# Performance work log

Hardware: AMD Instinct MI355X
Metric: run time of the kernel (lower is better)

The kernel has to match this reference:

```python
import jax, jax.numpy as jnp
import numpy as np

BETA = 0.25  # commitment cost


def setup_inputs() -> dict:
    key = jax.random.key(0)
    k1, k2 = jax.random.split(key)
    z = jax.random.normal(k1, (16, 512, 64, 64), dtype=jnp.float32)       # (B, C=e_dim, H, W)
    codebook = jax.random.normal(k2, (1024, 512), dtype=jnp.float32)      # (n_e, e_dim)
    return {"z": z, "codebook": codebook}


def reference(z, codebook):
    b, c, h, w = z.shape
    zp = jnp.transpose(z, (0, 2, 3, 1))                                   # (B, H, W, C)
    zf = zp.reshape(-1, c)                                                # (N, e_dim)

    d = (jnp.sum(zf * zf, axis=1, keepdims=True)
         + jnp.sum(codebook * codebook, axis=1)
         - 2.0 * (zf @ codebook.T))                                       # (N, n_e)
    idx = jnp.argmin(d, axis=1)                                           # (N,)

    # one-hot @ codebook == direct gather
    z_q = codebook[idx].reshape(zp.shape)                                 # (B, H, W, C)

    sg = jax.lax.stop_gradient
    e_latent_loss = jnp.mean((sg(z_q) - zp) ** 2)
    q_latent_loss = jnp.mean((z_q - sg(zp)) ** 2)
    codebook_loss = q_latent_loss + BETA * e_latent_loss

    # straight-through estimator
    z_q_st = zp + sg(z_q - zp)
    z_q_out = jnp.transpose(z_q_st, (0, 3, 1, 2))                         # (B, C, H, W)
    return z_q_out, codebook_loss, idx.reshape(b, 1, h, w)
```

## Files before the change

### kernel.cpp

```cpp
#include <hip/hip_runtime.h>
#include <hip/hip_bf16.h>


typedef _Float16 h8 __attribute__((ext_vector_type(8)));
typedef float f32x16 __attribute__((ext_vector_type(16)));

#define OUT_LOSS  33554432
#define OUT_IDX   33554433
#define MARGIN_T  0.15f

__device__ __forceinline__ void gload_lds16(const void* g, void* l) {
  __builtin_amdgcn_global_load_lds(
      (const __attribute__((address_space(1))) void*)g,
      (__attribute__((address_space(3))) void*)l, 16, 0, 0);
}

__global__ __launch_bounds__(64) void k0_prep(
    const float* __restrict__ cb, unsigned short* __restrict__ cb16,
    float* __restrict__ cnp, int* __restrict__ counters, float* __restrict__ loss_acc,
    int* __restrict__ idx_ws, unsigned long long* __restrict__ packed_ws)
{
  const int r = blockIdx.x, l = threadIdx.x;
  const float* row = cb + (size_t)r * 512;
  float4 a  = *(const float4*)(row + l * 8);
  float4 b4 = *(const float4*)(row + l * 8 + 4);
  h8 hv;
  hv[0] = (_Float16)a.x;  hv[1] = (_Float16)a.y;  hv[2] = (_Float16)a.z;  hv[3] = (_Float16)a.w;
  hv[4] = (_Float16)b4.x; hv[5] = (_Float16)b4.y; hv[6] = (_Float16)b4.z; hv[7] = (_Float16)b4.w;
  *reinterpret_cast<h8*>(cb16 + (size_t)r * 512 + l * 8) = hv;
  float s = a.x*a.x + a.y*a.y + a.z*a.z + a.w*a.w
          + b4.x*b4.x + b4.y*b4.y + b4.z*b4.z + b4.w*b4.w;
  #pragma unroll
  for (int off = 1; off < 64; off <<= 1) s += __shfl_xor(s, off);
  if (l == 0) {
    int jr = r & 31, ch = r >> 5;
    int khalf = (jr >> 2) & 1;
    int pat = jr - (khalf << 2);
    int rr  = (pat & 3) + ((pat >> 3) << 2);
    cnp[(ch << 5) + (khalf << 4) + rr] = 0.5f * s;
  }
  const int pix = (r << 6) + l;
  idx_ws[pix] = (int)0x80000000;
  packed_ws[pix] = ~0ull;
  if (r == 0 && l == 0) { counters[0] = 0; counters[1] = 0; *loss_acc = 0.f; }
}

__global__ __launch_bounds__(256, 2) void k1_main(
    const float* __restrict__ z, const unsigned short* __restrict__ cb16,
    const float* __restrict__ cnp,
    int* __restrict__ idx_ws, int* __restrict__ flaglist,
    unsigned long long* __restrict__ pairlist, int* __restrict__ counters)
{
  extern __shared__ char smem[];
  float* cn_lds = reinterpret_cast<float*>(smem + 65536);
  const int tid   = threadIdx.x;
  const int lane  = tid & 63;
  const int wave  = tid >> 6;
  const int pxl   = lane & 31;
  const int khalf = lane >> 5;
  const int px0   = blockIdx.x << 7;
  const int b     = px0 >> 12;
  const int hw0   = px0 & 4095;
  const int laneoff = pxl * 1024 + khalf * 16;

  {
    const char* src = reinterpret_cast<const char*>(cb16) + laneoff;
    #pragma unroll
    for (int i = 0; i < 8; ++i) {
      int slab = (wave << 3) + i;
      gload_lds16(src + slab * 32, smem + slab * 1024);
    }
  }

  h8 bfrag[32];
  {
    const float* zl = z + ((size_t)(b * 512 + khalf * 8)) * 4096 + hw0 + (wave << 5) + pxl;
    #pragma unroll
    for (int s = 0; s < 32; ++s) {
      const float* zs = zl + (size_t)s * 16 * 4096;
      h8 hv;
      #pragma unroll
      for (int e = 0; e < 8; ++e) hv[e] = (_Float16)zs[(size_t)e * 4096];
      bfrag[s] = hv;
    }
  }
  for (int i = tid; i < 1024; i += 256) cn_lds[i] = cnp[i];
  __syncthreads();

  float v0 = INFINITY, v1 = INFINITY, v2 = INFINITY, v3 = INFINITY;
  int   i0 = 0, i1 = 0, i2 = 0, i3 = 0;

  for (int ch = 0; ch < 32; ++ch) {
    const char* cbuf = smem + ((ch & 1) << 15);
    if (ch) {
      asm volatile("s_waitcnt vmcnt(0)" ::: "memory");
      __builtin_amdgcn_s_barrier();
    }
    if (ch < 31) {
      char* dbuf = smem + (((ch & 1) ^ 1) << 15);
      const char* src = reinterpret_cast<const char*>(cb16) + ((ch + 1) << 15) + laneoff;
      #pragma unroll
      for (int i = 0; i < 8; ++i) {
        int slab = (wave << 3) + i;
        gload_lds16(src + slab * 32, dbuf + slab * 1024);
      }
    }

    f32x16 acca, accb;
    #pragma unroll
    for (int i = 0; i < 16; ++i) { acca[i] = 0.f; accb[i] = 0.f; }
    {
      const char* ab = cbuf + (pxl << 4) + (khalf << 9);
      #pragma unroll
      for (int s = 0; s < 16; ++s) {
        h8 a0 = *reinterpret_cast<const h8*>(ab + (s << 10));
        h8 a1 = *reinterpret_cast<const h8*>(ab + ((s + 16) << 10));
        acca = __builtin_amdgcn_mfma_f32_32x32x16_f16(a0, bfrag[s],      acca, 0, 0, 0);
        accb = __builtin_amdgcn_mfma_f32_32x32x16_f16(a1, bfrag[s + 16], accb, 0, 0, 0);
      }
    }
    const float* cl = cn_lds + (ch << 5) + (khalf << 4);
    float4 q0 = *(const float4*)(cl);     float4 q1 = *(const float4*)(cl + 4);
    float4 q2 = *(const float4*)(cl + 8); float4 q3 = *(const float4*)(cl + 12);
    const float cn[16] = {q0.x,q0.y,q0.z,q0.w, q1.x,q1.y,q1.z,q1.w,
                          q2.x,q2.y,q2.z,q2.w, q3.x,q3.y,q3.z,q3.w};
    const int jbase = (ch << 5) + (khalf << 2);
    #pragma unroll
    for (int r = 0; r < 16; ++r) {
      int j = jbase + ((r & 3) + ((r >> 2) << 3));
      float sc = cn[r] - (acca[r] + accb[r]);
      if (__ballot(sc < v3)) {
        bool c0 = sc < v0, c1 = sc < v1, c2 = sc < v2, c3 = sc < v3;
        v3 = c2 ? v2 : (c3 ? sc : v3);  i3 = c2 ? i2 : (c3 ? j : i3);
        v2 = c1 ? v1 : (c2 ? sc : v2);  i2 = c1 ? i1 : (c2 ? j : i2);
        v1 = c0 ? v0 : (c1 ? sc : v1);  i1 = c0 ? i0 : (c1 ? j : i1);
        v0 = c0 ? sc : v0;              i0 = c0 ? j  : i0;
      }
    }
  }

  {
    float ow0 = __shfl_xor(v0, 32), ow1 = __shfl_xor(v1, 32),
          ow2 = __shfl_xor(v2, 32), ow3 = __shfl_xor(v3, 32);
    int   oj0 = __shfl_xor(i0, 32), oj1 = __shfl_xor(i1, 32),
          oj2 = __shfl_xor(i2, 32), oj3 = __shfl_xor(i3, 32);
    const float ow[4] = {ow0, ow1, ow2, ow3};
    const int   oj[4] = {oj0, oj1, oj2, oj3};
    #pragma unroll
    for (int k = 0; k < 4; ++k) {
      float ov = ow[k]; int oi = oj[k];
      bool c0 = ov < v0, c1 = ov < v1, c2 = ov < v2, c3 = ov < v3;
      v3 = c2 ? v2 : (c3 ? ov : v3);  i3 = c2 ? i2 : (c3 ? oi : i3);
      v2 = c1 ? v1 : (c2 ? ov : v2);  i2 = c1 ? i1 : (c2 ? oi : i2);
      v1 = c0 ? v0 : (c1 ? ov : v1);  i1 = c0 ? i0 : (c1 ? oi : i1);
      v0 = c0 ? ov : v0;              i0 = c0 ? oi : i0;
    }
  }

  const int pix = px0 + (wave << 5) + lane;
  bool sane = (v0 == v0) && (v3 == v3) && ((unsigned)i0 < 1024u);
  bool unfl = sane && (v1 - v0 >= MARGIN_T);
  bool quad = sane && !unfl && (v3 - v0 >= MARGIN_T);
  bool qpred = (lane < 32) && quad;
  bool fpred = (lane < 32) && !unfl && !quad;
  if (lane < 32) idx_ws[pix] = unfl ? i0 : (int)0x80000000;

  unsigned long long qm = __ballot(qpred);
  if (qm) {
    int leader = __ffsll(qm) - 1;
    int base = 0;
    if (lane == leader) base = atomicAdd(&counters[1], __popcll(qm));
    base = __shfl(base, leader);
    if (qpred) {
      int pos = __popcll(qm & ((1ull << lane) - 1ull));
      pairlist[base + pos] = (unsigned long long)(unsigned)pix
          | ((unsigned long long)(unsigned)i0 << 16)
          | ((unsigned long long)(unsigned)i1 << 26)
          | ((unsigned long long)(unsigned)i2 << 36)
          | ((unsigned long long)(unsigned)i3 << 46);
    }
  }
  unsigned long long fm = __ballot(fpred);
  if (fm) {
    int leader = __ffsll(fm) - 1;
    int base = 0;
    if (lane == leader) base = atomicAdd(&counters[0], __popcll(fm));
    base = __shfl(base, leader);
    if (fpred) {
      int pos = __popcll(fm & ((1ull << lane) - 1ull));
      flaglist[base + pos] = pix;
    }
  }
}

__global__ __launch_bounds__(256) void k2a_quad(
    const float* __restrict__ z, const float* __restrict__ cb,
    const unsigned long long* __restrict__ pairlist, const int* __restrict__ counters,
    int* __restrict__ idx_ws)
{
  const int lane = threadIdx.x & 63;
  const int wid  = (blockIdx.x << 2) + (threadIdx.x >> 6);
  const int nwav = gridDim.x << 2;
  const int nf   = counters[1];
  for (int e = wid; e < nf; e += nwav) {
    unsigned long long pk = pairlist[e];
    int pix = (int)(pk & 0xFFFFull);
    int c0 = (int)((pk >> 16) & 1023ull), c1 = (int)((pk >> 26) & 1023ull);
    int c2 = (int)((pk >> 36) & 1023ull), c3 = (int)((pk >> 46) & 1023ull);
    const float* zp = z + (size_t)(pix >> 12) * 512 * 4096 + (pix & 4095);
    double s0 = 0, s1 = 0, s2 = 0, s3 = 0;
    #pragma unroll
    for (int k = 0; k < 8; ++k) {
      int c = lane + (k << 6);
      double zv2 = 2.0 * (double)zp[(size_t)c * 4096];
      double a;
      a = (double)cb[(size_t)c0 * 512 + c]; s0 = fma(a, a - zv2, s0);
      a = (double)cb[(size_t)c1 * 512 + c]; s1 = fma(a, a - zv2, s1);
      a = (double)cb[(size_t)c2 * 512 + c]; s2 = fma(a, a - zv2, s2);
      a = (double)cb[(size_t)c3 * 512 + c]; s3 = fma(a, a - zv2, s3);
    }
    #pragma unroll
    for (int off = 32; off > 0; off >>= 1) {
      s0 += __shfl_xor(s0, off); s1 += __shfl_xor(s1, off);
      s2 += __shfl_xor(s2, off); s3 += __shfl_xor(s3, off);
    }
    double bv = s0; int bi = c0;
    if (s1 < bv || (s1 == bv && c1 < bi)) { bv = s1; bi = c1; }
    if (s2 < bv || (s2 == bv && c2 < bi)) { bv = s2; bi = c2; }
    if (s3 < bv || (s3 == bv && c3 < bi)) { bv = s3; bi = c3; }
    if (lane == 0) idx_ws[pix] = bi;
  }
}

__global__ __launch_bounds__(256) void k2_rescan(
    const float* __restrict__ z, const float* __restrict__ cb,
    const int* __restrict__ flaglist, const int* __restrict__ counters,
    unsigned long long* __restrict__ packed_ws)
{
  __shared__ float zb[16][512];
  __shared__ unsigned long long best[16];
  __shared__ int pixl[16];
  const int t = threadIdx.x;
  const int nflag = counters[0];
  const int ntasks = ((nflag + 15) >> 4) << 2;
  for (int task = blockIdx.x; task < ntasks; task += gridDim.x) {
    const int g = task >> 2, q = task & 3;
    int rem = nflag - (g << 4);
    const int npx = rem < 16 ? rem : 16;
    if (t < 16) {
      best[t] = ~0ull;
      pixl[t] = (t < npx) ? flaglist[(g << 4) + t] : 0;
    }
    __syncthreads();
    for (int i = t; i < (npx << 9); i += 256) {
      int p = i >> 9, c = i & 511;
      int pix = pixl[p];
      zb[p][c] = z[((size_t)(pix >> 12) * 512 + c) * 4096 + (pix & 4095)];
    }
    __syncthreads();
    const int j = (q << 8) + t;
    const float* row = cb + (size_t)j * 512;
    double dot[16];
    #pragma unroll
    for (int p = 0; p < 16; ++p) dot[p] = 0.0;
    double cn = 0.0;
    for (int k = 0; k < 512; k += 4) {
      float4 cv = *(const float4*)(row + k);
      double c0 = cv.x, c1 = cv.y, c2 = cv.z, c3 = cv.w;
      cn = fma(c0, c0, cn); cn = fma(c1, c1, cn);
      cn = fma(c2, c2, cn); cn = fma(c3, c3, cn);
      #pragma unroll
      for (int p = 0; p < 16; ++p) {
        dot[p] = fma(c0, (double)zb[p][k + 0], dot[p]);
        dot[p] = fma(c1, (double)zb[p][k + 1], dot[p]);
        dot[p] = fma(c2, (double)zb[p][k + 2], dot[p]);
        dot[p] = fma(c3, (double)zb[p][k + 3], dot[p]);
      }
    }
    #pragma unroll
    for (int p = 0; p < 16; ++p) {
      if (p < npx) {
        double d = fma(-2.0, dot[p], cn);
        unsigned long long u = (unsigned long long)__double_as_longlong(d);
        u = (u >> 63) ? ~u : (u | 0x8000000000000000ull);
        unsigned long long pkk = (u & ~1023ull) | (unsigned long long)j;
        atomicMin(&best[p], pkk);
      }
    }
    __syncthreads();
    if (t < npx) atomicMin(&packed_ws[pixl[t]], best[t]);
    __syncthreads();
  }
}

__global__ __launch_bounds__(256) void k3_out(
    const float* __restrict__ z, const float* __restrict__ cb,
    const int* __restrict__ idx_ws, const unsigned long long* __restrict__ packed_ws,
    float* __restrict__ out, float* __restrict__ loss_acc)
{
  extern __shared__ float rows[];
  __shared__ int idxs[32];
  __shared__ float wsum[4];
  const int t = threadIdx.x;
  const int pix0 = blockIdx.x << 5;
  const int b = pix0 >> 12, hw0 = pix0 & 4095;
  if (t < 32) {
    int pix = pix0 + t;
    int v = idx_ws[pix];
    unsigned j = (v < 0) ? (unsigned)(packed_ws[pix] & 1023ull) : (unsigned)v;
    j &= 1023u;
    idxs[t] = (int)j;
    out[OUT_IDX + pix] = (float)j;
  }
  __syncthreads();
  for (int i = t; i < 32 * 128; i += 256) {
    int r = i >> 7, kq = (i & 127) << 2;
    float4 v = *(const float4*)(cb + (size_t)idxs[r] * 512 + kq);
    float* dst = rows + r * 513 + kq;
    dst[0] = v.x; dst[1] = v.y; dst[2] = v.z; dst[3] = v.w;
  }
  __syncthreads();
  const int pl = (t & 7) << 2;
  const int cg = t >> 3;
  float acc = 0.f;
  for (int c0 = 0; c0 < 512; c0 += 32) {
    int c = c0 + cg;
    size_t go = ((size_t)(b * 512 + c)) * 4096 + hw0 + pl;
    float4 zv = *(const float4*)(z + go);
    float q0 = rows[(pl + 0) * 513 + c], q1 = rows[(pl + 1) * 513 + c];
    float q2 = rows[(pl + 2) * 513 + c], q3 = rows[(pl + 3) * 513 + c];
    float d0 = q0 - zv.x, d1 = q1 - zv.y, d2 = q2 - zv.z, d3 = q3 - zv.w;
    acc = fmaf(d0, d0, acc); acc = fmaf(d1, d1, acc);
    acc = fmaf(d2, d2, acc); acc = fmaf(d3, d3, acc);
    float4 qv;
    qv.x = zv.x + d0; qv.y = zv.y + d1;
    qv.z = zv.z + d2; qv.w = zv.w + d3;
    *reinterpret_cast<float4*>(out + go) = qv;
  }
  #pragma unroll
  for (int off = 32; off > 0; off >>= 1) acc += __shfl_down(acc, off);
  if ((t & 63) == 0) wsum[t >> 6] = acc;
  __syncthreads();
  if (t == 0) atomicAdd(loss_acc, wsum[0] + wsum[1] + wsum[2] + wsum[3]);
}

__global__ void k4_loss(const float* __restrict__ loss_acc, float* __restrict__ out)
{
  if (threadIdx.x == 0 && blockIdx.x == 0)
    out[OUT_LOSS] = loss_acc[0] * (1.25f / 33554432.f);
}

extern "C" void kernel_launch(void* const* d_in, const int* in_sizes, int n_in,
                              void* d_out, int out_size, void* d_ws, size_t ws_size,
                              hipStream_t stream) {
  const float* z  = (const float*)d_in[0];
  const float* cb = (const float*)d_in[1];
  float* out = (float*)d_out;
  char* ws = (char*)d_ws;
  unsigned short*      cb16      = (unsigned short*)(ws);
  float*               cnp       = (float*)(ws + 1048576);
  int*                 idx_ws    = (int*)(ws + 1052672);
  unsigned long long*  packed_ws = (unsigned long long*)(ws + 1314816);
  int*                 flaglist  = (int*)(ws + 1839104);
  unsigned long long*  pairlist  = (unsigned long long*)(ws + 2095360);
  int*                 counters  = (int*)(ws + 2619648);
  float*               loss_acc  = (float*)(ws + 2619656);

  (void)hipFuncSetAttribute((const void*)k1_main,
        hipFuncAttributeMaxDynamicSharedMemorySize, 69632);
  (void)hipFuncSetAttribute((const void*)k3_out,
        hipFuncAttributeMaxDynamicSharedMemorySize, 65664);

  k0_prep<<<1024, 64, 0, stream>>>(cb, cb16, cnp, counters, loss_acc, idx_ws, packed_ws);
  k1_main<<<512, 256, 69632, stream>>>(z, cb16, cnp, idx_ws, flaglist, pairlist, counters);
  k2a_quad<<<1024, 256, 0, stream>>>(z, cb, pairlist, counters, idx_ws);
  k2_rescan<<<256, 256, 0, stream>>>(z, cb, flaglist, counters, packed_ws);
  k3_out<<<2048, 256, 65664, stream>>>(z, cb, idx_ws, packed_ws, out, loss_acc);
  k4_loss<<<1, 1, 0, stream>>>(loss_acc, out);
}
```

Before: 183.9 us.

## Triple-buffer codebook half-chunks in LDS with two-stage-ahead prefetch in k1_main

The main distance kernel now streams each 32-code chunk as two 16 KB halves through a three-slot LDS ring, prefetching two stages ahead and waiting only on older loads (vmcnt(4)) instead of draining all loads each chunk. It uses a single MFMA accumulator chain with s_setprio around MFMA groups and does the top-4 update once per chunk, gated by a wave-wide min check. LDS per block drops from 68 KB to 52 KB. The aim is to hide global-to-LDS latency and cut barrier stalls, at the cost of twice as many barriers and a serial MFMA dependency chain.

Measured after the change: 431.3 us. +134.5%, slower.

```diff
diff --git a/kernel.cpp b/kernel.cpp
--- a/kernel.cpp
+++ b/kernel.cpp
@@ -52,7 +52,7 @@
     unsigned long long* __restrict__ pairlist, int* __restrict__ counters)
 {
   extern __shared__ char smem[];
-  float* cn_lds = reinterpret_cast<float*>(smem + 65536);
+  float* cn_lds = reinterpret_cast<float*>(smem + 49152);
   const int tid   = threadIdx.x;
   const int lane  = tid & 63;
   const int wave  = tid >> 6;
@@ -61,16 +61,17 @@
   const int px0   = blockIdx.x << 7;
   const int b     = px0 >> 12;
   const int hw0   = px0 & 4095;
+  const char* cbB = reinterpret_cast<const char*>(cb16);
   const int laneoff = pxl * 1024 + khalf * 16;
 
-  {
-    const char* src = reinterpret_cast<const char*>(cb16) + laneoff;
-    #pragma unroll
-    for (int i = 0; i < 8; ++i) {
-      int slab = (wave << 3) + i;
-      gload_lds16(src + slab * 32, smem + slab * 1024);
-    }
-  }
+  #pragma unroll
+  for (int i = 0; i < 4; ++i)
+    gload_lds16(cbB + laneoff + wave * 128 + i * 32,
+                smem + wave * 4096 + i * 1024);
+  #pragma unroll
+  for (int i = 0; i < 4; ++i)
+    gload_lds16(cbB + 512 + laneoff + wave * 128 + i * 32,
+                smem + 16384 + wave * 4096 + i * 1024);
 
   h8 bfrag[32];
   {
@@ -89,53 +90,70 @@
 
   float v0 = INFINITY, v1 = INFINITY, v2 = INFINITY, v3 = INFINITY;
   int   i0 = 0, i1 = 0, i2 = 0, i3 = 0;
-
-  for (int ch = 0; ch < 32; ++ch) {
-    const char* cbuf = smem + ((ch & 1) << 15);
-    if (ch) {
-      asm volatile("s_waitcnt vmcnt(0)" ::: "memory");
-      __builtin_amdgcn_s_barrier();
-    }
-    if (ch < 31) {
-      char* dbuf = smem + (((ch & 1) ^ 1) << 15);
-      const char* src = reinterpret_cast<const char*>(cb16) + ((ch + 1) << 15) + laneoff;
-      #pragma unroll
-      for (int i = 0; i < 8; ++i) {
-        int slab = (wave << 3) + i;
-        gload_lds16(src + slab * 32, dbuf + slab * 1024);
+  f32x16 acc;
+  #pragma unroll
+  for (int i = 0; i < 16; ++i) acc[i] = 0.f;
+
+  for (int st = 0; st < 64; ++st) {
+    const int h = st & 1;
+    const char* cbuf = smem + (st % 3) * 16384;
+    if (st < 63) { asm volatile("s_waitcnt vmcnt(4)" ::: "memory"); }
+    else         { asm volatile("s_waitcnt vmcnt(0)" ::: "memory"); }
+    __builtin_amdgcn_s_barrier();
+    __builtin_amdgcn_sched_barrier(0);
+
+    if (st + 2 < 64) {
+      const int c2 = (st + 2) >> 1, h2 = (st + 2) & 1;
+      char* dbuf = smem + ((st + 2) % 3) * 16384;
+      const char* src = cbB + c2 * 32768 + h2 * 512 + laneoff + wave * 128;
+      #pragma unroll
+      for (int i = 0; i < 4; ++i)
+        gload_lds16(src + i * 32, dbuf + wave * 4096 + i * 1024);
+    }
+
+    const char* ab = cbuf + (pxl << 4) + (khalf << 9);
+    #pragma unroll
+    for (int q = 0; q < 4; ++q) {
+      h8 a0 = *reinterpret_cast<const h8*>(ab + ((q * 4 + 0) << 10));
+      h8 a1 = *reinterpret_cast<const h8*>(ab + ((q * 4 + 1) << 10));
+      h8 a2 = *reinterpret_cast<const h8*>(ab + ((q * 4 + 2) << 10));
+      h8 a3 = *reinterpret_cast<const h8*>(ab + ((q * 4 + 3) << 10));
+      __builtin_amdgcn_s_setprio(1);
+      acc = __builtin_amdgcn_mfma_f32_32x32x16_f16(a0, bfrag[h * 16 + q * 4 + 0], acc, 0, 0, 0);
+      acc = __builtin_amdgcn_mfma_f32_32x32x16_f16(a1, bfrag[h * 16 + q * 4 + 1], acc, 0, 0, 0);
+      acc = __builtin_amdgcn_mfma_f32_32x32x16_f16(a2, bfrag[h * 16 + q * 4 + 2], acc, 0, 0, 0);
+      acc = __builtin_amdgcn_mfma_f32_32x32x16_f16(a3, bfrag[h * 16 + q * 4 + 3], acc, 0, 0, 0);
+      __builtin_amdgcn_s_setprio(0);
+    }
+
+    if (h) {
+      const int c = st >> 1;
+      const float* cl = cn_lds + (c << 5) + (khalf << 4);
+      float4 q0 = *(const float4*)(cl);     float4 q1 = *(const float4*)(cl + 4);
+      float4 q2 = *(const float4*)(cl + 8); float4 q3 = *(const float4*)(cl + 12);
+      const float cn[16] = {q0.x,q0.y,q0.z,q0.w, q1.x,q1.y,q1.z,q1.w,
+                            q2.x,q2.y,q2.z,q2.w, q3.x,q3.y,q3.z,q3.w};
+      float sc[16];
+      #pragma unroll
+      for (int r = 0; r < 16; ++r) sc[r] = cn[r] - acc[r];
+      float mn = sc[0];
+      #pragma unroll
+      for (int r = 1; r < 16; ++r) mn = fminf(mn, sc[r]);
+      if (__ballot(mn < v3)) {
+        const int jbase = (c << 5) + (khalf << 2);
+        #pragma unroll
+        for (int r = 0; r < 16; ++r) {
+          int j = jbase + ((r & 3) + ((r >> 2) << 3));
+          float s = sc[r];
+          bool c0 = s < v0, c1 = s < v1, c2 = s < v2, c3 = s < v3;
+          v3 = c2 ? v2 : (c3 ? s : v3);  i3 = c2 ? i2 : (c3 ? j : i3);
+          v2 = c1 ? v1 : (c2 ? s : v2);  i2 = c1 ? i1 : (c2 ? j : i2);
+          v1 = c0 ? v0 : (c1 ? s : v1);  i1 = c0 ? i0 : (c1 ? j : i1);
+          v0 = c0 ? s  : v0;             i0 = c0 ? j  : i0;
+        }
       }
-    }
-
-    f32x16 acca, accb;
-    #pragma unroll
-    for (int i = 0; i < 16; ++i) { acca[i] = 0.f; accb[i] = 0.f; }
-    {
-      const char* ab = cbuf + (pxl << 4) + (khalf << 9);
-      #pragma unroll
-      for (int s = 0; s < 16; ++s) {
-        h8 a0 = *reinterpret_cast<const h8*>(ab + (s << 10));
-        h8 a1 = *reinterpret_cast<const h8*>(ab + ((s + 16) << 10));
-        acca = __builtin_amdgcn_mfma_f32_32x32x16_f16(a0, bfrag[s],      acca, 0, 0, 0);
-        accb = __builtin_amdgcn_mfma_f32_32x32x16_f16(a1, bfrag[s + 16], accb, 0, 0, 0);
-      }
-    }
-    const float* cl = cn_lds + (ch << 5) + (khalf << 4);
-    float4 q0 = *(const float4*)(cl);     float4 q1 = *(const float4*)(cl + 4);
-    float4 q2 = *(const float4*)(cl + 8); float4 q3 = *(const float4*)(cl + 12);
-    const float cn[16] = {q0.x,q0.y,q0.z,q0.w, q1.x,q1.y,q1.z,q1.w,
-                          q2.x,q2.y,q2.z,q2.w, q3.x,q3.y,q3.z,q3.w};
-    const int jbase = (ch << 5) + (khalf << 2);
-    #pragma unroll
-    for (int r = 0; r < 16; ++r) {
-      int j = jbase + ((r & 3) + ((r >> 2) << 3));
-      float sc = cn[r] - (acca[r] + accb[r]);
-      if (__ballot(sc < v3)) {
-        bool c0 = sc < v0, c1 = sc < v1, c2 = sc < v2, c3 = sc < v3;
-        v3 = c2 ? v2 : (c3 ? sc : v3);  i3 = c2 ? i2 : (c3 ? j : i3);
-        v2 = c1 ? v1 : (c2 ? sc : v2);  i2 = c1 ? i1 : (c2 ? j : i2);
-        v1 = c0 ? v0 : (c1 ? sc : v1);  i1 = c0 ? i0 : (c1 ? j : i1);
-        v0 = c0 ? sc : v0;              i0 = c0 ? j  : i0;
-      }
+      #pragma unroll
+      for (int i = 0; i < 16; ++i) acc[i] = 0.f;
     }
   }
 
@@ -367,12 +385,12 @@
   float*               loss_acc  = (float*)(ws + 2619656);
 
   (void)hipFuncSetAttribute((const void*)k1_main,
-        hipFuncAttributeMaxDynamicSharedMemorySize, 69632);
+        hipFuncAttributeMaxDynamicSharedMemorySize, 53248);
   (void)hipFuncSetAttribute((const void*)k3_out,
         hipFuncAttributeMaxDynamicSharedMemorySize, 65664);
 
   k0_prep<<<1024, 64, 0, stream>>>(cb, cb16, cnp, counters, loss_acc, idx_ws, packed_ws);
-  k1_main<<<512, 256, 69632, stream>>>(z, cb16, cnp, idx_ws, flaglist, pairlist, counters);
+  k1_main<<<512, 256, 53248, stream>>>(z, cb16, cnp, idx_ws, flaglist, pairlist, counters);
   k2a_quad<<<1024, 256, 0, stream>>>(z, cb, pairlist, counters, idx_ws);
   k2_rescan<<<256, 256, 0, stream>>>(z, cb, flaglist, counters, packed_ws);
   k3_out<<<2048, 256, 65664, stream>>>(z, cb, idx_ws, packed_ws, out, loss_acc);
```
